# Kernel optimization log

Measured on AMD Instinct MI355X. Metric: run time of the kernel, lower is better.

The kernel has to match this reference:

```python
import jax, jax.numpy as jnp
import numpy as np

N_NODES = 100000
N_EDGES = 1600000
IN_DIM = 64
OUT_DIM = 64
HIDDEN = 64  # fixed in edge_weight_mlp
POS_DIM = 3


def setup_inputs() -> dict:
    key = jax.random.key(0)
    ks = jax.random.split(key, 10)
    x = jax.random.normal(ks[0], (N_NODES, IN_DIM), dtype=jnp.float32)
    edge_index = jax.random.randint(ks[1], (2, N_EDGES), 0, N_NODES, dtype=jnp.int64)
    pos = jax.random.normal(ks[2], (N_NODES, POS_DIM), dtype=jnp.float32)
    # edge_weight_mlp params: Linear(2*IN_DIM+1 -> 64), Linear(64 -> 1)
    s1 = 1.0 / np.sqrt(2 * IN_DIM + 1)
    w1 = jax.random.uniform(ks[3], (2 * IN_DIM + 1, HIDDEN), jnp.float32, -s1, s1)
    b1 = jax.random.uniform(ks[4], (HIDDEN,), jnp.float32, -s1, s1)
    s2 = 1.0 / np.sqrt(HIDDEN)
    w2 = jax.random.uniform(ks[5], (HIDDEN, 1), jnp.float32, -s2, s2)
    b2 = jax.random.uniform(ks[6], (1,), jnp.float32, -s2, s2)
    # transform: Linear(IN_DIM -> OUT_DIM)
    st = 1.0 / np.sqrt(IN_DIM)
    wt = jax.random.uniform(ks[7], (IN_DIM, OUT_DIM), jnp.float32, -st, st)
    bt = jax.random.uniform(ks[8], (OUT_DIM,), jnp.float32, -st, st)
    return {"x": x, "edge_index": edge_index, "pos": pos,
            "w1": w1, "b1": b1, "w2": w2, "b2": b2, "wt": wt, "bt": bt}


def reference(x, edge_index, pos, w1, b1, w2, b2, wt, bt):
    src, dst = edge_index[0], edge_index[1]
    # edge weights: MLP on [x_src, x_dst, |pos_dst - pos_src|]
    edge_length = jnp.linalg.norm(pos[dst] - pos[src], axis=1, keepdims=True)  # [E,1]
    edge_feat = jnp.concatenate([x[src], x[dst], edge_length], axis=1)  # [E, 2*in+1]
    h = jax.nn.relu(edge_feat @ w1 + b1)
    edge_weights = jax.nn.sigmoid(h @ w2 + b2)  # [E,1]
    # node transform, gather, weight, scatter-add
    x_t = x @ wt + bt  # [N, out]
    messages = x_t[src] * edge_weights  # [E, out]
    out = jax.ops.segment_sum(messages, dst, num_segments=x.shape[0])  # [N, out]
    return out, edge_weights
```

## Files before the change

### kernel.cpp

```cpp
#include <hip/hip_runtime.h>
#include <hip/hip_bf16.h>
#include <math.h>

#define NN 100000
#define NE 1600000
#define CAP 48
#define NB 391
#define BCAP 4608
#define EPB 4096
#define NBLKA ((NE + EPB - 1) / EPB)
#define NPREP ((NN + 63) / 64)
#define PSTR 72

typedef __attribute__((ext_vector_type(8))) short short8;
typedef __attribute__((ext_vector_type(4))) float floatx4;
typedef __attribute__((ext_vector_type(2))) float float2v;

#if __has_builtin(__builtin_elementwise_fma)
#define VFMA(a, b, c) __builtin_elementwise_fma((a), (b), (c))
#else
#define VFMA(a, b, c) ((a) * (b) + (c))
#endif

static __device__ __forceinline__ unsigned short f2bb(float f) {
    __hip_bfloat16 h = __float2bfloat16(f);
    return *(unsigned short*)&h;
}
static __device__ __forceinline__ float hi_f(unsigned u) {
    return __uint_as_float(u & 0xFFFF0000u);
}
static __device__ __forceinline__ float lo_f(unsigned u) {
    return __uint_as_float(u << 16);
}
static __device__ __forceinline__ float2v hi2(unsigned a, unsigned b) {
    float2v r; r.x = __uint_as_float(a & 0xFFFF0000u);
    r.y = __uint_as_float(b & 0xFFFF0000u); return r;
}
static __device__ __forceinline__ float2v lo2(unsigned a, unsigned b) {
    float2v r; r.x = __uint_as_float(a << 16);
    r.y = __uint_as_float(b << 16); return r;
}

__global__ __launch_bounds__(256) void init_kernel(
    const float* __restrict__ w1, const float* __restrict__ wt,
    unsigned short* __restrict__ wb, int* __restrict__ gcursor) {
    int t = threadIdx.x;
    if (blockIdx.x == 0) {
        for (int i = t; i < NB; i += 256) gcursor[i] = 0;
    }
    int stride = gridDim.x * 256;
    for (int idx = blockIdx.x * 256 + t; idx < 192 * 64; idx += stride) {
        int n = idx >> 6;
        int k = idx & 63;
        float v = (n < 64)  ? w1[(size_t)k * 64 + n]
                : (n < 128) ? w1[(size_t)(64 + k) * 64 + (n - 64)]
                            : wt[(size_t)k * 64 + (n - 128)];
        wb[idx] = f2bb(v);
    }
}

__global__ __launch_bounds__(256) void fused_prep_bucket(
    const float* __restrict__ x, const unsigned short* __restrict__ wb,
    const float* __restrict__ b1, const float* __restrict__ pos,
    const int* __restrict__ ei,
    unsigned int* __restrict__ rec, unsigned short* __restrict__ hd,
    float4* __restrict__ pos4, int* __restrict__ gcursor,
    uint2* __restrict__ bucketed) {
    __shared__ __align__(16) unsigned char smem[(64 + 192) * PSTR * 2];
    int t = threadIdx.x;
    if (blockIdx.x < NPREP) {
        unsigned short* As = (unsigned short*)smem;
        unsigned short* Bs = As + 64 * PSTR;
        int nbase = blockIdx.x * 64;
        {
            int r = t & 63;
            int node = nbase + r; if (node >= NN) node = NN - 1;
            const float4* xr = (const float4*)(x + (size_t)node * 64);
#pragma unroll
            for (int i = 0; i < 4; ++i) {
                int s = (t >> 6) + 4 * i;
                float4 v = xr[s];
                ushort4 o = {f2bb(v.x), f2bb(v.y), f2bb(v.z), f2bb(v.w)};
                *(ushort4*)&As[r * PSTR + s * 4] = o;
            }
        }
        {
            const uint4* wb4 = (const uint4*)wb;
#pragma unroll
            for (int i = 0; i < 6; ++i) {
                int v = t + 256 * i;
                uint4 q = wb4[v];
                int n = v >> 3;
                int k = (v & 7) * 8;
                *(uint4*)&Bs[n * PSTR + k] = q;
            }
        }
        if (t < 64) {
            int node = nbase + t;
            if (node < NN)
                pos4[node] = make_float4(pos[node * 3 + 0], pos[node * 3 + 1],
                                         pos[node * 3 + 2], 0.f);
        }
        __syncthreads();
        int lane = t & 63, wave = t >> 6;
        int grp = lane >> 4, l15 = lane & 15;
        floatx4 acc[12] = {};
        int arow = wave * 16 + l15;
#pragma unroll
        for (int ks = 0; ks < 2; ++ks) {
            int koff = ks * 32 + grp * 8;
            short8 a = *(const short8*)&As[arow * PSTR + koff];
#pragma unroll
            for (int nt = 0; nt < 12; ++nt) {
                short8 b = *(const short8*)&Bs[(nt * 16 + l15) * PSTR + koff];
                acc[nt] = __builtin_amdgcn_mfma_f32_16x16x32_bf16(a, b, acc[nt], 0, 0, 0);
            }
        }
#pragma unroll
        for (int nt = 0; nt < 4; ++nt) {
#pragma unroll
            for (int r = 0; r < 4; ++r) {
                int nr = wave * 16 + grp * 4 + r;
                int node = nbase + nr;
                if (node >= NN) continue;
                int col = nt * 16 + l15;
                rec[(size_t)node * 64 + col] =
                    ((unsigned)f2bb(acc[nt][r]) << 16) | f2bb(acc[8 + nt][r]);
                hd[(size_t)node * 64 + col] = f2bb(acc[4 + nt][r] + b1[col]);
            }
        }
    } else {
        int* cnt = (int*)smem;
        int* base_s = cnt + NB;
        for (int i = t; i < NB; i += 256) cnt[i] = 0;
        __syncthreads();
        int e0 = (blockIdx.x - NPREP) * EPB;
        unsigned int tags[16];
        int srcs[16], dsts[16];
#pragma unroll
        for (int i = 0; i < 16; ++i) {
            int e = e0 + i * 256 + t;
            tags[i] = 0xFFFFFFFFu;
            if (e < NE) {
                srcs[i] = ei[e];
                dsts[i] = ei[NE + e];
                int b = dsts[i] >> 8;
                int slot = atomicAdd(&cnt[b], 1);
                tags[i] = ((unsigned)b << 12) | (unsigned)slot;
            }
        }
        __syncthreads();
        for (int b = t; b < NB; b += 256)
            base_s[b] = atomicAdd(&gcursor[b], cnt[b]);
        __syncthreads();
#pragma unroll
        for (int i = 0; i < 16; ++i) {
            if (tags[i] != 0xFFFFFFFFu) {
                int e = e0 + i * 256 + t;
                int b = (int)(tags[i] >> 12);
                int slot = (int)(tags[i] & 0xFFFu);
                int p = base_s[b] + slot;
                if (p < BCAP) {
                    bucketed[(size_t)b * BCAP + p] =
                        make_uint2((unsigned)srcs[i] |
                                   (((unsigned)dsts[i] & 255u) << 17),
                                   (unsigned)e);
                }
            }
        }
    }
}

__global__ __launch_bounds__(1024) void csr_kernel(
    const uint2* __restrict__ bucketed, const int* __restrict__ gcursor,
    uint2* __restrict__ pairs, int* __restrict__ deg) {
    __shared__ int cur[256];
    int t = threadIdx.x;
    if (t < 256) cur[t] = 0;
    __syncthreads();
    int b = blockIdx.x;
    int n0 = b << 8;
    int cnt = gcursor[b];
    if (cnt > BCAP) cnt = BCAP;
    for (int i = t; i < cnt; i += 1024) {
        uint2 en = bucketed[(size_t)b * BCAP + i];
        int dwb = (int)((en.x >> 17) & 255u);
        unsigned src = en.x & 0x1FFFFu;
        int slot = atomicAdd(&cur[dwb], 1);
        if (slot < CAP)
            pairs[(size_t)(n0 + dwb) * CAP + slot] = make_uint2(src, en.y);
    }
    __syncthreads();
    if (t < 256) {
        int node = n0 + t;
        if (node < NN) deg[node] = (cur[t] > CAP) ? CAP : cur[t];
    }
}

__global__ __launch_bounds__(256) void mega_kernel(
    const uint2* __restrict__ pairs, const int* __restrict__ deg,
    const unsigned int* __restrict__ rec, const unsigned short* __restrict__ hd,
    const float4* __restrict__ pos4, const float* __restrict__ w1,
    const float* __restrict__ w2, const float* __restrict__ b2,
    const float* __restrict__ bt,
    float* __restrict__ ew_out, float* __restrict__ out) {
    int t = threadIdx.x;
    int w = t >> 6, lane = t & 63;
    int e8 = lane >> 3, hg = lane & 7;
    int node = blockIdx.x * 4 + w;
    if (node >= NN) return;

    const float2v zero2 = {0.f, 0.f};
    float2v a01 = zero2, a23 = zero2, a45 = zero2, a67 = zero2;
    float sw = 0.f;
    int d = deg[node];
    uint4 hz = ((const uint4*)(hd + (size_t)node * 64))[hg];
    float2v zb01 = {lo_f(hz.x), hi_f(hz.x)};
    float2v zb23 = {lo_f(hz.y), hi_f(hz.y)};
    float2v zb45 = {lo_f(hz.z), hi_f(hz.z)};
    float2v zb67 = {lo_f(hz.w), hi_f(hz.w)};
    const float2v* w2p = (const float2v*)(w2 + 8 * hg);
    float2v w20 = w2p[0], w21 = w2p[1], w22 = w2p[2], w23 = w2p[3];
    const float2v* wlp = (const float2v*)(w1 + 128 * 64 + 8 * hg);
    float2v wl0 = wlp[0], wl1 = wlp[1], wl2 = wlp[2], wl3 = wlp[3];
    float4 bta = ((const float4*)bt)[2 * hg];
    float4 btb = ((const float4*)bt)[2 * hg + 1];
    float4 pd = pos4[node];
    float b2v = b2[0];
    const uint2* seg = pairs + (size_t)node * CAP;
    const uint4* rec4 = (const uint4*)rec;

    if (d > 0) {
        int i0 = (e8 < d) ? e8 : (d - 1);
        uint2 pr_c = seg[i0];
        uint2 pr_n = pr_c;
        if (8 < d) { int i1 = (8 + e8 < d) ? (8 + e8) : (d - 1); pr_n = seg[i1]; }
        uint4 ua_c = rec4[(size_t)pr_c.x * 16 + 2 * hg];
        uint4 ub_c = rec4[(size_t)pr_c.x * 16 + 2 * hg + 1];
        float4 ps_c = pos4[pr_c.x];

#pragma unroll 2
        for (int j = 0; j < d; j += 8) {
            int jn = j + 8;
            uint2 pr_n2 = pr_n;
            uint4 ua_n = ua_c, ub_n = ub_c;
            float4 ps_n = ps_c;
            if (jn < d) {
                ua_n = rec4[(size_t)pr_n.x * 16 + 2 * hg];
                ub_n = rec4[(size_t)pr_n.x * 16 + 2 * hg + 1];
                ps_n = pos4[pr_n.x];
                if (jn + 8 < d) {
                    int i2 = (jn + 8 + e8 < d) ? (jn + 8 + e8) : (d - 1);
                    pr_n2 = seg[i2];
                }
            }
            bool valid = (j + e8 < d);
            float dx = pd.x - ps_c.x;
            float dy = pd.y - ps_c.y;
            float dz = pd.z - ps_c.z;
            float len = __builtin_amdgcn_sqrtf(dx * dx + dy * dy + dz * dz);
            float2v l2; l2.x = len; l2.y = len;
            float2v z, r, tp;
            z = zb01 + hi2(ua_c.x, ua_c.y); z = VFMA(l2, wl0, z);
            r = __builtin_elementwise_max(z, zero2); tp = r * w20;
            z = zb23 + hi2(ua_c.z, ua_c.w); z = VFMA(l2, wl1, z);
            r = __builtin_elementwise_max(z, zero2); tp = VFMA(r, w21, tp);
            z = zb45 + hi2(ub_c.x, ub_c.y); z = VFMA(l2, wl2, z);
            r = __builtin_elementwise_max(z, zero2); tp = VFMA(r, w22, tp);
            z = zb67 + hi2(ub_c.z, ub_c.w); z = VFMA(l2, wl3, z);
            r = __builtin_elementwise_max(z, zero2); tp = VFMA(r, w23, tp);
            float tt = tp.x + tp.y;
            tt += __shfl_xor(tt, 1);
            tt += __shfl_xor(tt, 2);
            tt += __shfl_xor(tt, 4);
            float ew = __builtin_amdgcn_rcpf(1.f + __expf(-(tt + b2v)));
            if (valid) {
                if (hg == 0) ew_out[pr_c.y] = ew;
                float2v e2; e2.x = ew; e2.y = ew;
                a01 = VFMA(e2, lo2(ua_c.x, ua_c.y), a01);
                a23 = VFMA(e2, lo2(ua_c.z, ua_c.w), a23);
                a45 = VFMA(e2, lo2(ub_c.x, ub_c.y), a45);
                a67 = VFMA(e2, lo2(ub_c.z, ub_c.w), a67);
                sw += ew;
            }
            pr_c = pr_n; pr_n = pr_n2;
            ua_c = ua_n; ub_c = ub_n; ps_c = ps_n;
        }
    }
    float acc0 = a01.x, acc1 = a01.y, acc2 = a23.x, acc3 = a23.y;
    float acc4 = a45.x, acc5 = a45.y, acc6 = a67.x, acc7 = a67.y;
#pragma unroll
    for (int off = 8; off < 64; off <<= 1) {
        acc0 += __shfl_xor(acc0, off);
        acc1 += __shfl_xor(acc1, off);
        acc2 += __shfl_xor(acc2, off);
        acc3 += __shfl_xor(acc3, off);
        acc4 += __shfl_xor(acc4, off);
        acc5 += __shfl_xor(acc5, off);
        acc6 += __shfl_xor(acc6, off);
        acc7 += __shfl_xor(acc7, off);
        sw   += __shfl_xor(sw, off);
    }
    if (e8 == 0) {
        float* orow = out + (size_t)node * 64 + hg * 8;
        float4 o1 = {acc0 + sw * bta.x, acc1 + sw * bta.y,
                     acc2 + sw * bta.z, acc3 + sw * bta.w};
        float4 o2 = {acc4 + sw * btb.x, acc5 + sw * btb.y,
                     acc6 + sw * btb.z, acc7 + sw * btb.w};
        *(float4*)orow = o1;
        *(float4*)(orow + 4) = o2;
    }
}

extern "C" void kernel_launch(void* const* d_in, const int* in_sizes, int n_in,
                              void* d_out, int out_size, void* d_ws, size_t ws_size,
                              hipStream_t stream) {
    const float* x   = (const float*)d_in[0];
    const int*   ei  = (const int*)d_in[1];
    const float* pos = (const float*)d_in[2];
    const float* w1  = (const float*)d_in[3];
    const float* b1  = (const float*)d_in[4];
    const float* w2  = (const float*)d_in[5];
    const float* b2  = (const float*)d_in[6];
    const float* wt  = (const float*)d_in[7];
    const float* bt  = (const float*)d_in[8];

    float* out    = (float*)d_out;
    float* ew_out = out + (size_t)NN * 64;

    unsigned int* rec = (unsigned int*)d_ws;
    unsigned short* hd = (unsigned short*)(rec + (size_t)NN * 64);
    uint2* pairs = (uint2*)(hd + (size_t)NN * 64);
    float4* pos4 = (float4*)(pairs + (size_t)NN * CAP);
    int* gcursor = (int*)(pos4 + NN);
    int* deg = gcursor + NB;
    unsigned short* wb = (unsigned short*)(deg + NN);

    uint2* bucketed = (uint2*)d_out;

    init_kernel<<<16, 256, 0, stream>>>(w1, wt, wb, gcursor);
    fused_prep_bucket<<<NPREP + NBLKA, 256, 0, stream>>>(
        x, wb, b1, pos, ei, rec, hd, pos4, gcursor, bucketed);
    csr_kernel<<<NB, 1024, 0, stream>>>(bucketed, gcursor, pairs, deg);
    mega_kernel<<<(NN + 3) / 4, 256, 0, stream>>>(pairs, deg, rec, hd, pos4,
                                                  w1, w2, b2, bt, ew_out, out);
}
```

Baseline: 236.6 us.

## Regroup stages: fuse weight prep with bucketing and node GEMM with CSR build

Kernels are regrouped: weight conversion now runs alongside edge bucketing in one launch, and the node-transform GEMM runs alongside the per-bucket CSR build in the next. The cursor reset becomes a memset. The CSR part drops from 1024-thread blocks to 256 threads, and bf16 packing uses the v_cvt_pk_bf16_f32 instruction. This removes one dependent launch and lets the GEMM overlap the CSR scatter. The risk is that the CSR blocks now have less parallelism per bucket.

```diff
diff --git a/kernel.cpp b/kernel.cpp
--- a/kernel.cpp
+++ b/kernel.cpp
@@ -26,6 +26,11 @@
     __hip_bfloat16 h = __float2bfloat16(f);
     return *(unsigned short*)&h;
 }
+static __device__ __forceinline__ unsigned cvt_pk_bf16(float lo, float hi) {
+    unsigned r;
+    asm("v_cvt_pk_bf16_f32 %0, %1, %2" : "=v"(r) : "v"(lo), "v"(hi));
+    return r;
+}
 static __device__ __forceinline__ float hi_f(unsigned u) {
     return __uint_as_float(u & 0xFFFF0000u);
 }
@@ -41,100 +46,28 @@
     r.y = __uint_as_float(b << 16); return r;
 }
 
-__global__ __launch_bounds__(256) void init_kernel(
+__global__ __launch_bounds__(256) void initbucket_kernel(
     const float* __restrict__ w1, const float* __restrict__ wt,
-    unsigned short* __restrict__ wb, int* __restrict__ gcursor) {
+    const int* __restrict__ ei,
+    unsigned short* __restrict__ wb, int* __restrict__ gcursor,
+    uint2* __restrict__ bucketed) {
+    __shared__ int cnt[NB];
+    __shared__ int base_s[NB];
     int t = threadIdx.x;
-    if (blockIdx.x == 0) {
-        for (int i = t; i < NB; i += 256) gcursor[i] = 0;
-    }
-    int stride = gridDim.x * 256;
-    for (int idx = blockIdx.x * 256 + t; idx < 192 * 64; idx += stride) {
-        int n = idx >> 6;
-        int k = idx & 63;
-        float v = (n < 64)  ? w1[(size_t)k * 64 + n]
-                : (n < 128) ? w1[(size_t)(64 + k) * 64 + (n - 64)]
-                            : wt[(size_t)k * 64 + (n - 128)];
-        wb[idx] = f2bb(v);
-    }
-}
-
-__global__ __launch_bounds__(256) void fused_prep_bucket(
-    const float* __restrict__ x, const unsigned short* __restrict__ wb,
-    const float* __restrict__ b1, const float* __restrict__ pos,
-    const int* __restrict__ ei,
-    unsigned int* __restrict__ rec, unsigned short* __restrict__ hd,
-    float4* __restrict__ pos4, int* __restrict__ gcursor,
-    uint2* __restrict__ bucketed) {
-    __shared__ __align__(16) unsigned char smem[(64 + 192) * PSTR * 2];
-    int t = threadIdx.x;
-    if (blockIdx.x < NPREP) {
-        unsigned short* As = (unsigned short*)smem;
-        unsigned short* Bs = As + 64 * PSTR;
-        int nbase = blockIdx.x * 64;
-        {
-            int r = t & 63;
-            int node = nbase + r; if (node >= NN) node = NN - 1;
-            const float4* xr = (const float4*)(x + (size_t)node * 64);
-#pragma unroll
-            for (int i = 0; i < 4; ++i) {
-                int s = (t >> 6) + 4 * i;
-                float4 v = xr[s];
-                ushort4 o = {f2bb(v.x), f2bb(v.y), f2bb(v.z), f2bb(v.w)};
-                *(ushort4*)&As[r * PSTR + s * 4] = o;
-            }
-        }
-        {
-            const uint4* wb4 = (const uint4*)wb;
-#pragma unroll
-            for (int i = 0; i < 6; ++i) {
-                int v = t + 256 * i;
-                uint4 q = wb4[v];
-                int n = v >> 3;
-                int k = (v & 7) * 8;
-                *(uint4*)&Bs[n * PSTR + k] = q;
-            }
-        }
-        if (t < 64) {
-            int node = nbase + t;
-            if (node < NN)
-                pos4[node] = make_float4(pos[node * 3 + 0], pos[node * 3 + 1],
-                                         pos[node * 3 + 2], 0.f);
-        }
-        __syncthreads();
-        int lane = t & 63, wave = t >> 6;
-        int grp = lane >> 4, l15 = lane & 15;
-        floatx4 acc[12] = {};
-        int arow = wave * 16 + l15;
-#pragma unroll
-        for (int ks = 0; ks < 2; ++ks) {
-            int koff = ks * 32 + grp * 8;
-            short8 a = *(const short8*)&As[arow * PSTR + koff];
-#pragma unroll
-            for (int nt = 0; nt < 12; ++nt) {
-                short8 b = *(const short8*)&Bs[(nt * 16 + l15) * PSTR + koff];
-                acc[nt] = __builtin_amdgcn_mfma_f32_16x16x32_bf16(a, b, acc[nt], 0, 0, 0);
-            }
-        }
-#pragma unroll
-        for (int nt = 0; nt < 4; ++nt) {
-#pragma unroll
-            for (int r = 0; r < 4; ++r) {
-                int nr = wave * 16 + grp * 4 + r;
-                int node = nbase + nr;
-                if (node >= NN) continue;
-                int col = nt * 16 + l15;
-                rec[(size_t)node * 64 + col] =
-                    ((unsigned)f2bb(acc[nt][r]) << 16) | f2bb(acc[8 + nt][r]);
-                hd[(size_t)node * 64 + col] = f2bb(acc[4 + nt][r] + b1[col]);
-            }
+    if (blockIdx.x < 16) {
+        int stride = 16 * 256;
+        for (int idx = blockIdx.x * 256 + t; idx < 192 * 64; idx += stride) {
+            int n = idx >> 6;
+            int k = idx & 63;
+            float v = (n < 64)  ? w1[(size_t)k * 64 + n]
+                    : (n < 128) ? w1[(size_t)(64 + k) * 64 + (n - 64)]
+                                : wt[(size_t)k * 64 + (n - 128)];
+            wb[idx] = f2bb(v);
         }
     } else {
-        int* cnt = (int*)smem;
-        int* base_s = cnt + NB;
         for (int i = t; i < NB; i += 256) cnt[i] = 0;
         __syncthreads();
-        int e0 = (blockIdx.x - NPREP) * EPB;
+        int e0 = (blockIdx.x - 16) * EPB;
         unsigned int tags[16];
         int srcs[16], dsts[16];
 #pragma unroll
@@ -171,27 +104,94 @@
     }
 }
 
-__global__ __launch_bounds__(1024) void csr_kernel(
+__global__ __launch_bounds__(256) void prepcsr_kernel(
+    const float* __restrict__ x, const unsigned short* __restrict__ wb,
+    const float* __restrict__ b1, const float* __restrict__ pos,
     const uint2* __restrict__ bucketed, const int* __restrict__ gcursor,
-    uint2* __restrict__ pairs, int* __restrict__ deg) {
-    __shared__ int cur[256];
+    unsigned int* __restrict__ rec, unsigned short* __restrict__ hd,
+    float4* __restrict__ pos4, uint2* __restrict__ pairs,
+    int* __restrict__ deg) {
+    __shared__ __align__(16) unsigned char smem[(64 + 192) * PSTR * 2];
     int t = threadIdx.x;
-    if (t < 256) cur[t] = 0;
-    __syncthreads();
-    int b = blockIdx.x;
-    int n0 = b << 8;
-    int cnt = gcursor[b];
-    if (cnt > BCAP) cnt = BCAP;
-    for (int i = t; i < cnt; i += 1024) {
-        uint2 en = bucketed[(size_t)b * BCAP + i];
-        int dwb = (int)((en.x >> 17) & 255u);
-        unsigned src = en.x & 0x1FFFFu;
-        int slot = atomicAdd(&cur[dwb], 1);
-        if (slot < CAP)
-            pairs[(size_t)(n0 + dwb) * CAP + slot] = make_uint2(src, en.y);
-    }
-    __syncthreads();
-    if (t < 256) {
+    if (blockIdx.x < NPREP) {
+        unsigned short* As = (unsigned short*)smem;
+        unsigned short* Bs = As + 64 * PSTR;
+        int nbase = blockIdx.x * 64;
+        {
+            int r = t & 63;
+            int node = nbase + r; if (node >= NN) node = NN - 1;
+            const float4* xr = (const float4*)(x + (size_t)node * 64);
+#pragma unroll
+            for (int i = 0; i < 4; ++i) {
+                int s = (t >> 6) + 4 * i;
+                float4 v = xr[s];
+                *(uint2*)&As[r * PSTR + s * 4] =
+                    make_uint2(cvt_pk_bf16(v.x, v.y), cvt_pk_bf16(v.z, v.w));
+            }
+        }
+        {
+            const uint4* wb4 = (const uint4*)wb;
+#pragma unroll
+            for (int i = 0; i < 6; ++i) {
+                int v = t + 256 * i;
+                uint4 q = wb4[v];
+                int n = v >> 3;
+                int k = (v & 7) * 8;
+                *(uint4*)&Bs[n * PSTR + k] = q;
+            }
+        }
+        if (t < 64) {
+            int node = nbase + t;
+            if (node < NN)
+                pos4[node] = make_float4(pos[node * 3 + 0], pos[node * 3 + 1],
+                                         pos[node * 3 + 2], 0.f);
+        }
+        __syncthreads();
+        int lane = t & 63, wave = t >> 6;
+        int grp = lane >> 4, l15 = lane & 15;
+        floatx4 acc[12] = {};
+        int arow = wave * 16 + l15;
+#pragma unroll
+        for (int ks = 0; ks < 2; ++ks) {
+            int koff = ks * 32 + grp * 8;
+            short8 a = *(const short8*)&As[arow * PSTR + koff];
+#pragma unroll
+            for (int nt = 0; nt < 12; ++nt) {
+                short8 b = *(const short8*)&Bs[(nt * 16 + l15) * PSTR + koff];
+                acc[nt] = __builtin_amdgcn_mfma_f32_16x16x32_bf16(a, b, acc[nt], 0, 0, 0);
+            }
+        }
+#pragma unroll
+        for (int nt = 0; nt < 4; ++nt) {
+            int col = nt * 16 + l15;
+            float b1v = b1[col];
+#pragma unroll
+            for (int r = 0; r < 4; ++r) {
+                int nr = wave * 16 + grp * 4 + r;
+                int node = nbase + nr;
+                if (node >= NN) continue;
+                rec[(size_t)node * 64 + col] =
+                    cvt_pk_bf16(acc[8 + nt][r], acc[nt][r]);
+                hd[(size_t)node * 64 + col] = f2bb(acc[4 + nt][r] + b1v);
+            }
+        }
+    } else {
+        int* cur = (int*)smem;
+        cur[t] = 0;
+        __syncthreads();
+        int b = blockIdx.x - NPREP;
+        int n0 = b << 8;
+        int cnt = gcursor[b];
+        if (cnt > BCAP) cnt = BCAP;
+        for (int i = t; i < cnt; i += 256) {
+            uint2 en = bucketed[(size_t)b * BCAP + i];
+            int dwb = (int)((en.x >> 17) & 255u);
+            unsigned src = en.x & 0x1FFFFu;
+            int slot = atomicAdd(&cur[dwb], 1);
+            if (slot < CAP)
+                pairs[(size_t)(n0 + dwb) * CAP + slot] = make_uint2(src, en.y);
+        }
+        __syncthreads();
         int node = n0 + t;
         if (node < NN) deg[node] = (cur[t] > CAP) ? CAP : cur[t];
     }
@@ -338,10 +338,11 @@
 
     uint2* bucketed = (uint2*)d_out;
 
-    init_kernel<<<16, 256, 0, stream>>>(w1, wt, wb, gcursor);
-    fused_prep_bucket<<<NPREP + NBLKA, 256, 0, stream>>>(
-        x, wb, b1, pos, ei, rec, hd, pos4, gcursor, bucketed);
-    csr_kernel<<<NB, 1024, 0, stream>>>(bucketed, gcursor, pairs, deg);
+    hipMemsetAsync(gcursor, 0, NB * sizeof(int), stream);
+    initbucket_kernel<<<16 + NBLKA, 256, 0, stream>>>(
+        w1, wt, ei, wb, gcursor, bucketed);
+    prepcsr_kernel<<<NPREP + NB, 256, 0, stream>>>(
+        x, wb, b1, pos, bucketed, gcursor, rec, hd, pos4, pairs, deg);
     mega_kernel<<<(NN + 3) / 4, 256, 0, stream>>>(pairs, deg, rec, hd, pos4,
                                                   w1, w2, b2, bt, ew_out, out);
 }
```

Result: slower. 241.5 us (+2.1%).
